# Kernel optimization log

Hardware: AMD Instinct MI355X
Metric: run time of the kernel (lower is better)

The kernel has to match this reference:

```python
import jax, jax.numpy as jnp
import numpy as np

B, T, V = 256, 40, 5000
D, Z, L = 512, 128, 2


def setup_inputs() -> dict:
    key = jax.random.key(0)
    ks = jax.random.split(key, 10)
    s = 0.05  # weight scale to keep gates unsaturated
    return {
        "z": jax.random.normal(ks[0], (B, Z), jnp.float32),
        "x": jax.random.randint(ks[1], (B, T), 0, V),
        "emb": jax.random.normal(ks[2], (V, D), jnp.float32) * s,
        "Wg0": jax.random.normal(ks[3], (4, D, D + Z + D), jnp.float32) * s,
        "bg0": jnp.zeros((4, D), jnp.float32),
        "Wg1": jax.random.normal(ks[4], (4, D, D + D), jnp.float32) * s,
        "bg1": jnp.zeros((4, D), jnp.float32),
        "Wout": jax.random.normal(ks[5], (V, D + Z), jnp.float32) * s,
        "bout": jnp.zeros((V,), jnp.float32),
        "tw1": jax.random.normal(ks[6], (L, 4 * D, Z), jnp.float32) * s,
        "tb1": jnp.zeros((L, 4 * D), jnp.float32),
        "tw2": jax.random.normal(ks[7], (L, 2 * D, 4 * D), jnp.float32) * s,
        "tb2": jnp.zeros((L, 2 * D), jnp.float32),
    }


def reference(z, x, emb, Wg0, bg0, Wg1, bg1, Wout, bout, tw1, tb1, tw2, tb2):
    b, d = z.shape[0], emb.shape[1]
    # transformh0: Linear -> ReLU -> Linear -> Tanh, then split into (h0, c0)
    states = []
    for l in range(L):
        hh = jnp.tanh(jax.nn.relu(z @ tw1[l].T + tb1[l]) @ tw2[l].T + tb2[l])
        hh = hh.reshape(b, 2, d)
        states.append((hh[:, 0], hh[:, 1]))
    states = tuple(states)

    emb_x = emb[x]  # [B, T, D]
    Ws, bs = (Wg0, Wg1), (bg0, bg1)

    def cell(xin, h, c, W, bb):
        hx = jnp.concatenate([h, xin], axis=-1)  # Gate cats [h, input]
        g = jnp.einsum('bf,gdf->bgd', hx, W) + bb  # fused 4 gate GEMMs
        i = jax.nn.sigmoid(g[:, 0])
        f = jax.nn.sigmoid(g[:, 1])
        o = jax.nn.sigmoid(g[:, 2])
        cn = jnp.tanh(g[:, 3])
        c = f * c + i * cn
        return o * jnp.tanh(c), c

    def multi(xin, states):
        H = jnp.zeros((b, d), xin.dtype)
        new, cur = [], xin
        for l in range(L):
            h, c = cell(cur, states[l][0], states[l][1], Ws[l], bs[l])
            H = H + h
            new.append((h, c))
            cur = h
        return H, tuple(new)

    h_t, states = multi(jnp.concatenate([emb_x[:, 0], z], axis=-1), states)

    def step(carry, inp):
        h_t, states = carry
        e_i, x_i = inp
        logits = jnp.concatenate([h_t, z], axis=-1) @ Wout.T + bout
        lp = jax.nn.log_softmax(logits, axis=-1)
        lp_i = jnp.take_along_axis(lp, x_i[:, None], axis=-1)  # [B,1]
        h_t, states = multi(jnp.concatenate([e_i, z], axis=-1), states)
        return (h_t, states), lp_i

    xs = (jnp.swapaxes(emb_x[:, 1:], 0, 1), x[:, 1:].T)
    _, lps = jax.lax.scan(step, (h_t, states), xs)
    # cumsum over time then take last == sum over steps -> [B, 1]
    return jnp.sum(lps, axis=0)
```

## Files before the change

kernel.cpp:

```cpp
#include <hip/hip_runtime.h>


typedef unsigned int uint;
typedef unsigned short ushort;
typedef unsigned long long u64;
typedef __attribute__((ext_vector_type(8))) __bf16 bf16x8;
typedef __attribute__((ext_vector_type(4))) float f32x4;
typedef __attribute__((ext_vector_type(8))) ushort ushort8v;

#define OFF_CNT 0L
#define OFF_W0  4096L
#define OFF_W1  4722688L
#define OFF_WO  8916992L
#define OFF_EFT 15470592L
#define OFF_ZFT 25956352L
#define OFF_TW1 26021888L
#define OFF_TW2 27070464L
#define OFF_GB  35459072L
#define OFF_C0  40701952L
#define OFF_C1  41226240L
#define OFF_MB  41750528L
#define OFF_SB  41914368L
#define OFF_TGT 42078208L
#define OFF_H0S 42205184L
#define OFF_H1S 52690944L
#define OFF_HSS 63176704L

#define HPAR 262144L
#define HMT  131072L
#define SLOT_G 24576
#define SLOT_L 32768


__device__ __forceinline__ uint ald32(const uint* p) {
  return __hip_atomic_load(p, __ATOMIC_RELAXED, __HIP_MEMORY_SCOPE_AGENT);
}
__device__ __forceinline__ void ast32(uint* p, uint v) {
  __hip_atomic_store(p, v, __ATOMIC_RELAXED, __HIP_MEMORY_SCOPE_AGENT);
}
__device__ __forceinline__ float aldf(const float* p) {
  return __hip_atomic_load(p, __ATOMIC_RELAXED, __HIP_MEMORY_SCOPE_AGENT);
}
__device__ __forceinline__ void astf(float* p, float v) {
  __hip_atomic_store(p, v, __ATOMIC_RELAXED, __HIP_MEMORY_SCOPE_AGENT);
}
__device__ __forceinline__ void ast64(u64* p, u64 v) {
  __hip_atomic_store(p, v, __ATOMIC_RELAXED, __HIP_MEMORY_SCOPE_AGENT);
}

__device__ __forceinline__ void postS(uint* s, uint v) {
  __syncthreads();
  if (threadIdx.x == 0) ast32(s, v);
}

__device__ __forceinline__ void gateM(const uint* S, int n, u64 need, uint tgt, uint& vc) {
  if (threadIdx.x < 64) {
    const int li = threadIdx.x;
    uint v = (li < n) ? vc : 0xffffffffu;
    int r = 0;
    for (;;) {
      if ((__ballot((int)(v >= tgt)) & need) == need) break;
      if (li < n && v < tgt) v = ald32(S + li);
      if ((__ballot((int)(v >= tgt)) & need) == need) break;
      if (r < 2) __builtin_amdgcn_s_sleep(1);
      else if (r < 5) __builtin_amdgcn_s_sleep(4);
      else __builtin_amdgcn_s_sleep(8);
      ++r;
    }
    if (li < n) vc = v;
  }
  asm volatile("" ::: "memory");
  __builtin_amdgcn_s_barrier();
  asm volatile("" ::: "memory");
}

__device__ __forceinline__ ushort f2bf(float f) {
  uint u = __float_as_uint(f);
  u = (u + 0x7fffu + ((u >> 16) & 1u)) >> 16;
  return (ushort)u;
}
__device__ __forceinline__ float bf2f(ushort u) { return __uint_as_float(((uint)u) << 16); }
__device__ __forceinline__ float sigm(float v) { return 1.f / (1.f + __expf(-v)); }
__device__ __forceinline__ float tanh_f(float v) {
  float a = fabsf(v);
  float e = __expf(-2.f * a);
  return copysignf((1.f - e) / (1.f + e), v);
}
__device__ __forceinline__ f32x4 mfma16(bf16x8 a, bf16x8 b, f32x4 c) {
  return __builtin_amdgcn_mfma_f32_16x16x32_bf16(a, b, c, 0, 0, 0);
}

__device__ __forceinline__ long fta(int b, int k, int KC) {
  return ((long)(((b >> 7) & 1) * KC + (k >> 5)) << 12) +
         (((((b >> 4) & 7) << 2) + ((k >> 3) & 3)) << 7) + ((b & 15) << 3) + (k & 7);
}

__device__ __forceinline__ void gl_lds16(const char* g, char* l) {
  __builtin_amdgcn_global_load_lds((const __attribute__((address_space(1))) void*)g,
                                   (__attribute__((address_space(3))) void*)l, 16, 0, 0);
}

__device__ __forceinline__ void stageA4(const char* A, char* dst, int o) {
#pragma unroll
  for (int i = 0; i < 4; ++i) gl_lds16(A + i * 4096 + o, dst + i * 4096 + o);
}
__device__ __forceinline__ void stage_gB(int bsec, const char* Bs, char* dst, int o) {
  const char* B = Bs + (long)bsec * 8192;
#pragma unroll
  for (int i = 0; i < 2; ++i) gl_lds16(B + i * 4096 + o, dst + 16384 + i * 4096 + o);
}
__device__ __forceinline__ void stage_lB(int bsec, const char* Blo, const char* Bhi, char* dst,
                                         int o) {
  const char* bl = Blo + (long)bsec * 8192;
  const char* bh = Bhi + (long)bsec * 8192;
#pragma unroll
  for (int i = 0; i < 2; ++i) gl_lds16(bl + i * 4096 + o, dst + 16384 + i * 4096 + o);
#pragma unroll
  for (int i = 0; i < 2; ++i) gl_lds16(bh + i * 4096 + o, dst + 24576 + i * 4096 + o);
}

__device__ __forceinline__ void gw3(int r) {
  if (r <= 0) __builtin_amdgcn_s_waitcnt(0x0F70);
  else if (r == 1) __builtin_amdgcn_s_waitcnt(0x0F76);
  else if (r == 2) __builtin_amdgcn_s_waitcnt(0x0F7C);
  else __builtin_amdgcn_s_waitcnt(0x4F72);
}
__device__ __forceinline__ void lw2(int r) {
  if (r <= 0) __builtin_amdgcn_s_waitcnt(0x0F70);
  else if (r == 1) __builtin_amdgcn_s_waitcnt(0x0F78);
  else __builtin_amdgcn_s_waitcnt(0x4F70);
}
__device__ __forceinline__ void gvw16(int s) {
  if (s == 0) __builtin_amdgcn_s_waitcnt(0x4F78);
  else if (s <= 12) __builtin_amdgcn_s_waitcnt(0x4F72);
  else if (s == 13) __builtin_amdgcn_s_waitcnt(0x0F7C);
  else if (s == 14) __builtin_amdgcn_s_waitcnt(0x0F76);
  else __builtin_amdgcn_s_waitcnt(0x0F70);
}

__device__ __forceinline__ void gemm_chunk_g(const char* sb, int ab, int bb, f32x4 (&acc)[4][2]) {
#pragma unroll
  for (int c = 0; c < 2; ++c) {
    const char* ap = sb + c * 8192 + ab;
    const char* bp = sb + c * 4096 + bb;
    bf16x8 Af0 = *(const bf16x8*)(ap);
    bf16x8 Af1 = *(const bf16x8*)(ap + 1024);
    bf16x8 Af2 = *(const bf16x8*)(ap + 2048);
    bf16x8 Af3 = *(const bf16x8*)(ap + 3072);
    bf16x8 Bf0 = *(const bf16x8*)(bp);
    bf16x8 Bf1 = *(const bf16x8*)(bp + 1024);
    acc[0][0] = mfma16(Af0, Bf0, acc[0][0]);
    acc[0][1] = mfma16(Af0, Bf1, acc[0][1]);
    acc[1][0] = mfma16(Af1, Bf0, acc[1][0]);
    acc[1][1] = mfma16(Af1, Bf1, acc[1][1]);
    acc[2][0] = mfma16(Af2, Bf0, acc[2][0]);
    acc[2][1] = mfma16(Af2, Bf1, acc[2][1]);
    acc[3][0] = mfma16(Af3, Bf0, acc[3][0]);
    acc[3][1] = mfma16(Af3, Bf1, acc[3][1]);
  }
}

__device__ __forceinline__ void gemm_chunk_l(const char* sb, int ab, int bb, f32x4 (&acc)[4][4]) {
#pragma unroll
  for (int c = 0; c < 2; ++c) {
    const char* ap = sb + c * 8192 + ab;
    const char* bp = sb + c * 4096 + bb;
    bf16x8 Af[4], Bf[4];
#pragma unroll
    for (int m = 0; m < 4; ++m) Af[m] = *(const bf16x8*)(ap + m * 1024);
#pragma unroll
    for (int n = 0; n < 4; ++n) Bf[n] = *(const bf16x8*)(bp + n * 1024);
#pragma unroll
    for (int m = 0; m < 4; ++m)
#pragma unroll
      for (int n = 0; n < 4; ++n) acc[m][n] = mfma16(Af[m], Bf[n], acc[m][n]);
  }
}

__device__ __forceinline__ void phaseL8(const char* A0, const char* Blo, const char* Bhi,
                                        char* smem, int o, int ab, int bb, f32x4 (&acc)[4][4]) {
#pragma unroll
  for (int p = 0; p < 4; ++p) {
    char* d = smem + p * SLOT_L;
    stageA4(A0 + (long)p * 16384, d, o);
    stage_lB(p, Blo, Bhi, d, o);
  }
#pragma unroll
  for (int s = 0; s < 8; ++s) {
    if (s == 0) __builtin_amdgcn_s_waitcnt(0x4F78);
    else if (s <= 5) __builtin_amdgcn_s_waitcnt(0x4F70);
    else if (s == 6) __builtin_amdgcn_s_waitcnt(0x0F78);
    else __builtin_amdgcn_s_waitcnt(0x0F70);
    __builtin_amdgcn_s_barrier();
    if (s >= 1 && s <= 4) {
      const int sn = s + 3;
      char* d = smem + (sn % 4) * SLOT_L;
      stageA4(A0 + (long)sn * 16384, d, o);
      stage_lB(sn, Blo, Bhi, d, o);
    }
    gemm_chunk_l(smem + (s % 4) * SLOT_L, ab, bb, acc);
  }
  __builtin_amdgcn_s_barrier();
}

__device__ __forceinline__ void run_gemm_init(const char* A0, const char* Bs, int S, char* smem,
                                              int tid, int wm, int wn, int lane,
                                              f32x4 (&acc)[4][2]) {
  const int o = tid * 16;
  const int D = S < 4 ? S : 4;
  for (int s = 0; s < D; ++s) {
    char* d = smem + s * SLOT_G;
    stageA4(A0 + (long)s * 16384, d, o);
    stage_gB(s, Bs, d, o);
  }
  const int ab = wm * 4096 + lane * 16;
  const int bb = 16384 + wn * 2048 + lane * 16;
  for (int s = 0; s < S; ++s) {
    const int rem = S - 1 - s;
    gw3(rem < 3 ? rem : 3);
    __builtin_amdgcn_s_barrier();
    char* sb = smem + (s % 5) * SLOT_G;
    if (s + 4 < S) {
      char* d = smem + ((s + 4) % 5) * SLOT_G;
      stageA4(A0 + (long)(s + 4) * 16384, d, o);
      stage_gB(s + 4, Bs, d, o);
    }
    gemm_chunk_g(sb, ab, bb, acc);
  }
  __syncthreads();
}

__device__ __forceinline__ void store_lds_tile(float* lds, f32x4 (&acc)[4][2], int wm, int wn,
                                               int lane) {
  const int l15 = lane & 15, lq = lane >> 4;
#pragma unroll
  for (int m = 0; m < 4; ++m)
#pragma unroll
    for (int n = 0; n < 2; ++n)
#pragma unroll
      for (int r = 0; r < 4; ++r)
        lds[(wm * 64 + m * 16 + lq * 4 + r) * 68 + (wn * 32 + n * 16 + l15)] = acc[m][n][r];
}
__device__ __forceinline__ void store_lds_tile128(float* lds, f32x4 (&acc)[4][4], int wm, int wn,
                                                  int lane) {
  const int l15 = lane & 15, lq = lane >> 4;
#pragma unroll
  for (int m = 0; m < 4; ++m)
#pragma unroll
    for (int n = 0; n < 4; ++n)
#pragma unroll
      for (int r = 0; r < 4; ++r)
        lds[(wm * 64 + m * 16 + lq * 4 + r) * 132 + (wn * 64 + n * 16 + l15)] = acc[m][n][r];
}

template <bool WHS>
__device__ __forceinline__ void gates_pw4(const float* tile, int tid, int b0, int d0,
                                          const float* __restrict__ bg, float (&cp)[8],
                                          ushort* __restrict__ hw, const uint (&h0p)[4],
                                          ushort* __restrict__ hs) {
#pragma unroll
  for (int jj = 0; jj < 4; ++jj) {
    const int pi = tid + jj * 256;
    const int bl = pi >> 3, e = pi & 7;
    const f32x4 g0 = ((const f32x4*)tile)[bl * 17 + 2 * e];
    const f32x4 g1 = ((const f32x4*)tile)[bl * 17 + 2 * e + 1];
    const int d = d0 + 2 * e, b = b0 + bl;
    float h2[2];
#pragma unroll
    for (int u = 0; u < 2; ++u) {
      const f32x4 g = u ? g1 : g0;
      const int dd = d + u;
      const float ii = sigm(g[0] + bg[dd]);
      const float ff = sigm(g[1] + bg[512 + dd]);
      const float oo = sigm(g[2] + bg[1024 + dd]);
      const float cn = tanh_f(g[3] + bg[1536 + dd]);
      const float c = ff * cp[jj * 2 + u] + ii * cn;
      cp[jj * 2 + u] = c;
      h2[u] = oo * tanh_f(c);
    }
    const long ft = fta(b, d, 16);
    ast32((uint*)(hw + ft), (uint)f2bf(h2[0]) | ((uint)f2bf(h2[1]) << 16));
    if (WHS) {
      const uint h0v = h0p[jj];
      const float s0 = h2[0] + bf2f((ushort)(h0v & 0xffffu));
      const float s1 = h2[1] + bf2f((ushort)(h0v >> 16));
      ast32((uint*)(hs + ft), (uint)f2bf(s0) | ((uint)f2bf(s1) << 16));
    }
  }
}

__device__ __forceinline__ float combine_row4(const float* __restrict__ MBc,
                                              const float* __restrict__ SBc,
                                              const float* __restrict__ TGTc, int r, int lane) {
  float M = lane < 40 ? aldf(&MBc[r * 40 + lane]) : -3.0e38f;
  float S = lane < 40 ? aldf(&SBc[r * 40 + lane]) : 0.f;
#pragma unroll
  for (int off = 32; off > 0; off >>= 1) {
    const float Mo = __shfl_xor(M, off, 64);
    const float So = __shfl_xor(S, off, 64);
    const float Mn = fmaxf(M, Mo);
    S = S * __expf(M - Mn) + So * __expf(Mo - Mn);
    M = Mn;
  }
  return aldf(&TGTc[r]) - (M + __logf(S));
}

__device__ __forceinline__ void cv8(ushort8v& o, const float* s) {
  const f32x4 a = *(const f32x4*)s, b = *(const f32x4*)(s + 4);
#pragma unroll
  for (int j = 0; j < 4; ++j) o[j] = f2bf(a[j]);
#pragma unroll
  for (int j = 0; j < 4; ++j) o[4 + j] = f2bf(b[j]);
}
__device__ __forceinline__ void bft8(ushort* dst, int col, int kg, int KC, const float* src) {
  ushort8v o;
  cv8(o, src);
  *(ushort8v*)(dst + ((long)((col >> 6) * KC + (kg >> 2)) << 11) +
               (((((col >> 4) & 3) << 2) + (kg & 3)) << 7) + ((col & 15) << 3)) = o;
}
__device__ __forceinline__ void bft8z(ushort* dst, int col, int kg, int KC) {
  ushort8v o = (ushort8v)0;
  *(ushort8v*)(dst + ((long)((col >> 6) * KC + (kg >> 2)) << 11) +
               (((((col >> 4) & 3) << 2) + (kg & 3)) << 7) + ((col & 15) << 3)) = o;
}
__device__ __forceinline__ void aft8(ushort* dst, int b, int kg, int KC, const float* src) {
  ushort8v o;
  cv8(o, src);
  *(ushort8v*)(dst + ((long)(((b >> 7) & 1) * KC + (kg >> 2)) << 12) +
               (((((b >> 4) & 7) << 2) + (kg & 3)) << 7) + ((b & 15) << 3)) = o;
}

__global__ void __launch_bounds__(256) prep_kernel(
    const float* __restrict__ Wg0, const float* __restrict__ Wg1, const float* __restrict__ Wout,
    const float* __restrict__ emb, const float* __restrict__ z, const int* __restrict__ x,
    const float* __restrict__ tw1, const float* __restrict__ tw2, unsigned char* __restrict__ ws) {
  ushort* W0 = (ushort*)(ws + OFF_W0);
  ushort* W1 = (ushort*)(ws + OFF_W1);
  ushort* WO = (ushort*)(ws + OFF_WO);
  ushort* EF = (ushort*)(ws + OFF_EFT);
  ushort* ZF = (ushort*)(ws + OFF_ZFT);
  ushort* T1 = (ushort*)(ws + OFF_TW1);
  ushort* T2 = (ushort*)(ws + OFF_TW2);
  const long N0 = 294912, N1 = 262144, N2 = 409600, N3 = 655360, N4 = 4096, N5 = 65536,
             N6 = 524288;
  const long total = N0 + N1 + N2 + N3 + N4 + N5 + N6;
  for (long idx = (long)blockIdx.x * 256 + threadIdx.x; idx < total;
       idx += (long)gridDim.x * 256) {
    long j = idx;
    if (j < N0) {
      const int col = (int)(j / 144), kg = (int)(j - (long)col * 144);
      bft8(W0, col, kg, 36, Wg0 + (long)((col & 3) * 512 + (col >> 2)) * 1152 + kg * 8);
    } else if ((j -= N0) < N1) {
      const int col = (int)(j >> 7), kg = (int)(j & 127);
      bft8(W1, col, kg, 32, Wg1 + (long)((col & 3) * 512 + (col >> 2)) * 1024 + kg * 8);
    } else if ((j -= N1) < N2) {
      const int col = (int)(j / 80), kg = (int)(j - (long)col * 80);
      if (col < 5000)
        bft8(WO, col, kg, 20, Wout + (long)col * 640 + kg * 8);
      else
        bft8z(WO, col, kg, 20);
    } else if ((j -= N2) < N3) {
      const int t = (int)(j >> 14), r = (int)(j & 16383);
      const int b = r >> 6, kg = r & 63;
      aft8(EF + (long)t * 131072, b, kg, 16, emb + (long)x[b * 40 + t] * 512 + kg * 8);
    } else if ((j -= N3) < N4) {
      const int b = (int)(j >> 4), kg = (int)(j & 15);
      aft8(ZF, b, kg, 4, z + b * 128 + kg * 8);
    } else if ((j -= N4) < N5) {
      const int col = (int)(j >> 4), kg = (int)(j & 15);
      bft8(T1, col, kg, 4, tw1 + (long)(col >> 11) * 262144 + (long)(col & 2047) * 128 + kg * 8);
    } else {
      j -= N5;
      const int col = (int)(j >> 8), kg = (int)(j & 255);
      bft8(T2, col, kg, 64, tw2 + (long)(col >> 10) * 2097152 + (long)(col & 1023) * 2048 + kg * 8);
    }
  }
}

__global__ void __launch_bounds__(256) decoder_main(
    const int* __restrict__ x, const float* __restrict__ bg0, const float* __restrict__ bg1,
    const float* __restrict__ bout, const float* __restrict__ tb1, const float* __restrict__ tb2,
    unsigned char* __restrict__ ws, float* __restrict__ out) {
  __shared__ __align__(16) char smem[157696];

  uint* CNT = (uint*)(ws + OFF_CNT);

  const char* cW0 = (const char*)(ws + OFF_W0);
  const char* cW1 = (const char*)(ws + OFF_W1);
  const char* cWO = (const char*)(ws + OFF_WO);
  const char* cEF = (const char*)(ws + OFF_EFT);
  const char* cZF = (const char*)(ws + OFF_ZFT);
  const char* cT1 = (const char*)(ws + OFF_TW1);
  const char* cT2 = (const char*)(ws + OFF_TW2);
  char* cGB = (char*)(ws + OFF_GB);
  char* cH0S = (char*)(ws + OFF_H0S);
  char* cH1S = (char*)(ws + OFF_H1S);
  char* cHSS = (char*)(ws + OFF_HSS);
  float* C0f = (float*)(ws + OFF_C0);
  float* C1f = (float*)(ws + OFF_C1);
  float* MBf = (float*)(ws + OFF_MB);
  float* SBf = (float*)(ws + OFF_SB);
  float* TGTf = (float*)(ws + OFF_TGT);

  const int bid = blockIdx.x;
  const int tid = threadIdx.x;
  const int lane = tid & 63;
  const int w = tid >> 6;
  const int wm = w & 1, wn = w >> 1;
  const int xcd = bid & 7;
  const int slot = bid >> 3;
  const int o16 = tid * 16;

  int role, mt_r = 0, idx = 0;
  if (xcd < 2) {
    role = 0; mt_r = xcd; idx = slot;
  } else if (xcd < 4) {
    role = 1; mt_r = xcd - 2; idx = slot;
  } else if (xcd < 6) {
    role = 2; mt_r = xcd - 4; idx = slot;
  } else if (slot < 8) {
    role = 2; mt_r = xcd - 6; idx = 32 + slot;
  } else if (slot < 24) {
    role = 3; idx = (xcd - 6) * 16 + (slot - 8); mt_r = idx >> 4;
  } else {
    return;
  }

  const int ab = wm * 4096 + lane * 16;
  const int bbg = 16384 + wn * 2048 + lane * 16;
  const int bbl = 16384 + wn * 8192 + lane * 16;
  float* EPI = (float*)(smem + 122880);

  float cpriv[8];
  float accO0 = 0.f, accO1 = 0.f;

  if (bid < 128) {
    const int i_mt = bid & 1, i_ng = bid >> 1;
    f32x4 acc[4][2];
#pragma unroll
    for (int m = 0; m < 4; ++m)
#pragma unroll
      for (int n = 0; n < 2; ++n) acc[m][n] = (f32x4){0.f, 0.f, 0.f, 0.f};
    run_gemm_init(cZF + (long)i_mt * 32768, cT1 + (long)i_ng * 16384, 2, smem, tid, wm, wn,
                  lane, acc);
    store_lds_tile(EPI, acc, wm, wn, lane);
    __syncthreads();
    const int b0i = i_mt * 128, n0i = i_ng * 64;
    ushort* GBu = (ushort*)cGB;
    for (int i = tid; i < 2048; i += 256) {
      const int bl = i >> 4, q = i & 15;
      const f32x4 v = ((const f32x4*)EPI)[bl * 17 + q];
      const int cb = n0i + q * 4;
      const int l = cb >> 11, rr = cb & 2047;
      u64 pk = 0;
#pragma unroll
      for (int cc = 0; cc < 4; ++cc) pk |= (u64)f2bf(fmaxf(v[cc] + tb1[cb + cc], 0.f)) << (cc * 16);
      ast64((u64*)(GBu + (long)l * 524288 + fta(b0i + bl, rr, 64)), pk);
    }
    postS(CNT + 512 + bid, 1u);
  }

  if (bid < 64) {
    uint ca = 0, cb2 = 0;
    gateM(CNT + 512, 64, ~0ull, 1u, ca);
    gateM(CNT + 576, 64, ~0ull, 1u, cb2);
    const int i_mt = bid & 1, i_ng = bid >> 1;
    const int l = i_ng >> 4;
    f32x4 acc[4][2];
#pragma unroll
    for (int m = 0; m < 4; ++m)
#pragma unroll
      for (int n = 0; n < 2; ++n) acc[m][n] = (f32x4){0.f, 0.f, 0.f, 0.f};
    run_gemm_init(cGB + (long)l * 1048576 + (long)i_mt * 524288, cT2 + (long)i_ng * 262144, 32,
                  smem, tid, wm, wn, lane, acc);
    store_lds_tile(EPI, acc, wm, wn, lane);
    __syncthreads();
    const int b0i = i_mt * 128, n0i = i_ng * 64;
    for (int i = tid; i < 2048; i += 256) {
      const int bl = i >> 4, q = i & 15;
      const f32x4 v = ((const f32x4*)EPI)[bl * 17 + q];
      const int cb = n0i + q * 4;
      const int ll = cb >> 10, rr = cb & 1023;
      const int b = b0i + bl;
      if (rr < 512) {
        u64 pk = 0;
#pragma unroll
        for (int cc = 0; cc < 4; ++cc) pk |= (u64)f2bf(tanh_f(v[cc] + tb2[cb + cc])) << (cc * 16);
        ast64((u64*)((ushort*)(ll ? cH1S : cH0S) + fta(b, rr, 16)), pk);
      } else {
        float* Cf = (ll ? C1f : C0f) + b * 512 + (rr - 512);
#pragma unroll
        for (int cc = 0; cc < 4; ++cc) astf(Cf + cc, tanh_f(v[cc] + tb2[cb + cc]));
      }
    }
    postS(CNT + 640 + bid, 1u);
  }

  if (role == 0) {
    const int mt = mt_r, g = idx;
    uint* SH0m = CNT + mt * 64;
    const char* Az = cZF + (long)mt * 32768;
    const char* Bs = cW0 + (long)g * 147456;
    f32x4 pz0[4][2];
#pragma unroll
    for (int m = 0; m < 4; ++m)
#pragma unroll
      for (int n = 0; n < 2; ++n) pz0[m][n] = (f32x4){0.f, 0.f, 0.f, 0.f};
    run_gemm_init(Az, Bs + 131072, 2, smem, tid, wm, wn, lane, pz0);
    uint cI2 = 0, ch0 = 0;
    gateM(CNT + 640, 64, ~0ull, 1u, cI2);
#pragma unroll
    for (int jj = 0; jj < 4; ++jj) {
      const int pi = tid + jj * 256, bl = pi >> 3, e = pi & 7;
      cpriv[jj * 2 + 0] = aldf(&C0f[(mt * 128 + bl) * 512 + g * 16 + 2 * e]);
      cpriv[jj * 2 + 1] = aldf(&C0f[(mt * 128 + bl) * 512 + g * 16 + 2 * e + 1]);
    }
    uint dum[4] = {0, 0, 0, 0};
    for (int t = 0; t < 39; ++t) {
      const char* Ae = cEF + (long)t * HPAR + (long)mt * HMT;
      const char* Ah = cH0S + (long)t * HPAR + (long)mt * HMT;
      if (t >= 1) gateM(SH0m, 32, 0xFFFFFFFFull, (uint)t, ch0);
      f32x4 acc[4][2];
#pragma unroll
      for (int m = 0; m < 4; ++m)
#pragma unroll
        for (int n = 0; n < 2; ++n) acc[m][n] = pz0[m][n];
#pragma unroll
      for (int p = 0; p < 5; ++p) {
        char* d = smem + p * SLOT_G;
        stageA4(Ae + (long)p * 16384, d, o16);
        stage_gB(8 + p, Bs, d, o16);
      }
      for (int s = 0; s < 16; ++s) {
        gvw16(s);
        __builtin_amdgcn_s_barrier();
        const int sn = s + 4;
        if (s >= 1 && sn < 16) {
          char* d = smem + (sn % 5) * SLOT_G;
          if (sn < 8) {
            stageA4(Ae + (long)sn * 16384, d, o16);
            stage_gB(8 + sn, Bs, d, o16);
          } else {
            stageA4(Ah + (long)(sn - 8) * 16384, d, o16);
            stage_gB(sn - 8, Bs, d, o16);
          }
        }
        gemm_chunk_g(smem + (s % 5) * SLOT_G, ab, bbg, acc);
      }
      store_lds_tile(EPI, acc, wm, wn, lane);
      __syncthreads();
      gates_pw4<false>(EPI, tid, mt * 128, g * 16, bg0, cpriv,
                       (ushort*)(cH0S + (long)(t + 1) * HPAR), dum, nullptr);
      postS(&SH0m[g], (uint)(t + 1));
    }
  } else if (role == 1) {
    const int mt = mt_r, g = idx;
    uint* SH0m = CNT + mt * 64;
    uint* SH1m = CNT + 128 + mt * 64;
    const char* Bs = cW1 + (long)g * 131072;
    uint cI2 = 0, ch1 = 0, ch0 = 0;
    gateM(CNT + 640, 64, ~0ull, 1u, cI2);
#pragma unroll
    for (int jj = 0; jj < 4; ++jj) {
      const int pi = tid + jj * 256, bl = pi >> 3, e = pi & 7;
      cpriv[jj * 2 + 0] = aldf(&C1f[(mt * 128 + bl) * 512 + g * 16 + 2 * e]);
      cpriv[jj * 2 + 1] = aldf(&C1f[(mt * 128 + bl) * 512 + g * 16 + 2 * e + 1]);
    }
    for (int t = 0; t < 39; ++t) {
      const char* Ah1 = cH1S + (long)t * HPAR + (long)mt * HMT;
      const char* Ah0 = cH0S + (long)(t + 1) * HPAR + (long)mt * HMT;
      if (t >= 1) gateM(SH1m, 32, 0xFFFFFFFFull, (uint)t, ch1);
      gateM(SH0m, 32, 0xFFFFFFFFull, (uint)(t + 1), ch0);
      f32x4 acc[4][2];
#pragma unroll
      for (int m = 0; m < 4; ++m)
#pragma unroll
        for (int n = 0; n < 2; ++n) acc[m][n] = (f32x4){0.f, 0.f, 0.f, 0.f};
#pragma unroll
      for (int p = 0; p < 5; ++p) {
        char* d = smem + p * SLOT_G;
        stageA4(Ah1 + (long)p * 16384, d, o16);
        stage_gB(p, Bs, d, o16);
      }
      for (int s = 0; s < 16; ++s) {
        gvw16(s);
        __builtin_amdgcn_s_barrier();
        const int sn = s + 4;
        if (s >= 1 && sn < 16) {
          char* d = smem + (sn % 5) * SLOT_G;
          const char* A = sn < 8 ? Ah1 + (long)sn * 16384 : Ah0 + (long)(sn - 8) * 16384;
          stageA4(A, d, o16);
          stage_gB(sn, Bs, d, o16);
        }
        gemm_chunk_g(smem + (s % 5) * SLOT_G, ab, bbg, acc);
      }
      uint h0p[4];
      {
        const ushort* h0r = (const ushort*)(cH0S + (long)(t + 1) * HPAR);
#pragma unroll
        for (int jj = 0; jj < 4; ++jj) {
          const int pi = tid + jj * 256, bl = pi >> 3, e = pi & 7;
          h0p[jj] = *(const uint*)(h0r + fta(mt * 128 + bl, g * 16 + 2 * e, 16));
        }
      }
      store_lds_tile(EPI, acc, wm, wn, lane);
      __syncthreads();
      gates_pw4<true>(EPI, tid, mt * 128, g * 16, bg1, cpriv,
                      (ushort*)(cH1S + (long)(t + 1) * HPAR), h0p,
                      (ushort*)(cHSS + (long)t * HPAR));
      postS(&SH1m[g], (uint)(t + 1));
    }
  } else if (role == 2) {
    const int lmt = mt_r, lng = idx;
    uint* SH1m = CNT + 128 + lmt * 64;
    uint* SLGm = CNT + 256 + lmt * 64;
    uint* SCBm = CNT + 384 + lmt * 64;
    const char* Blo = cWO + (long)(2 * lng) * 81920;
    const char* Bhi = cWO + (long)(2 * lng + 1) * 81920;
    const char* Az = cZF + (long)lmt * 32768;
    f32x4 pz[4][4];
#pragma unroll
    for (int m = 0; m < 4; ++m)
#pragma unroll
      for (int n = 0; n < 4; ++n) pz[m][n] = (f32x4){0.f, 0.f, 0.f, 0.f};
#pragma unroll
    for (int p = 0; p < 2; ++p) {
      char* d = smem + p * SLOT_L;
      stageA4(Az + (long)p * 16384, d, o16);
      stage_lB(8 + p, Blo, Bhi, d, o16);
    }
    for (int s = 0; s < 2; ++s) {
      lw2(1 - s);
      __builtin_amdgcn_s_barrier();
      gemm_chunk_l(smem + s * SLOT_L, ab, bbl, pz);
    }
    __syncthreads();
    {
      const int l15 = lane & 15;
#pragma unroll
      for (int n = 0; n < 4; ++n) {
        const int col = lng * 128 + wn * 64 + n * 16 + l15;
        const float bb = col < 5000 ? bout[col] : -3.0e38f;
#pragma unroll
        for (int m = 0; m < 4; ++m)
#pragma unroll
          for (int r = 0; r < 4; ++r) pz[m][n][r] += bb;
      }
    }
    uint ch1 = 0, ccb = 0;
    for (int t = 0; t < 39; ++t) {
      const char* Ahs = cHSS + (long)t * HPAR + (long)lmt * HMT;
      if (t >= 4) gateM(SCBm, 16, 0xFFFFull, (uint)(t - 3), ccb);
      gateM(SH1m, 32, 0xFFFFFFFFull, (uint)(t + 1), ch1);
      f32x4 acc[4][4];
#pragma unroll
      for (int m = 0; m < 4; ++m)
#pragma unroll
        for (int n = 0; n < 4; ++n) acc[m][n] = pz[m][n];
      phaseL8(Ahs, Blo, Bhi, smem, o16, ab, bbl, acc);
      __syncthreads();
      store_lds_tile128((float*)smem, acc, wm, wn, lane);
      __syncthreads();
      const int row = tid >> 1, half = tid & 1, b = lmt * 128 + row;
      const int n0 = lng * 128 + half * 64;
      const int xt = x[b * 40 + t + 1];
      const float* rowp = (const float*)smem + row * 132 + half * 64;
      float mx = -3.0e38f, tv = 0.f;
      for (int j = 0; j < 64; j += 4) {
        const f32x4 v = *(const f32x4*)(rowp + j);
#pragma unroll
        for (int cc = 0; cc < 4; ++cc) {
          mx = fmaxf(mx, v[cc]);
          if (n0 + j + cc == xt) tv = v[cc];
        }
      }
      float sa = 0.f;
      for (int j = 0; j < 64; j += 4) {
        const f32x4 v = *(const f32x4*)(rowp + j);
#pragma unroll
        for (int cc = 0; cc < 4; ++cc) sa += __expf(v[cc] - mx);
      }
      const float mo = __shfl_xor(mx, 1, 64), so = __shfl_xor(sa, 1, 64),
                  to = __shfl_xor(tv, 1, 64);
      const float Mn = fmaxf(mx, mo);
      const float Sm = sa * __expf(mx - Mn) + so * __expf(mo - Mn);
      const int sl = t & 3;
      if (half == 0) {
        astf(&MBf[sl * 10240 + b * 40 + lng], Mn);
        astf(&SBf[sl * 10240 + b * 40 + lng], Sm);
        if (xt >= lng * 128 && xt < lng * 128 + 128) astf(&TGTf[sl * 256 + b], tv + to);
      }
      postS(&SLGm[lng], (uint)(t + 1));
    }
  } else {
    const int cb = idx;
    const int cmt = mt_r;
    uint* SLGm = CNT + 256 + cmt * 64;
    uint* SCBm = CNT + 384 + cmt * 64;
    const int r0 = cb * 8 + w * 2;
    uint clg = 0;
    for (int t = 0; t < 39; ++t) {
      gateM(SLGm, 40, (1ull << 40) - 1, (uint)(t + 1), clg);
      const int sl = t & 3;
      accO0 += combine_row4(MBf + sl * 10240, SBf + sl * 10240, TGTf + sl * 256, r0, lane);
      accO1 += combine_row4(MBf + sl * 10240, SBf + sl * 10240, TGTf + sl * 256, r0 + 1, lane);
      postS(&SCBm[cb & 15], (uint)(t + 1));
    }
    if (lane == 0) {
      out[r0] = accO0;
      out[r0 + 1] = accO1;
    }
  }
}

extern "C" void kernel_launch(void* const* d_in, const int* in_sizes, int n_in, void* d_out,
                              int out_size, void* d_ws, size_t ws_size, hipStream_t stream) {
  const float* z = (const float*)d_in[0];
  const int* x = (const int*)d_in[1];
  const float* emb = (const float*)d_in[2];
  const float* Wg0 = (const float*)d_in[3];
  const float* bg0 = (const float*)d_in[4];
  const float* Wg1 = (const float*)d_in[5];
  const float* bg1 = (const float*)d_in[6];
  const float* Wout = (const float*)d_in[7];
  const float* bout = (const float*)d_in[8];
  const float* tw1 = (const float*)d_in[9];
  const float* tb1 = (const float*)d_in[10];
  const float* tw2 = (const float*)d_in[11];
  const float* tb2 = (const float*)d_in[12];
  unsigned char* ws = (unsigned char*)d_ws;
  float* out = (float*)d_out;

  hipMemsetAsync(ws, 0, 4096, stream);
  prep_kernel<<<2048, 256, 0, stream>>>(Wg0, Wg1, Wout, emb, z, x, tw1, tw2, ws);
  decoder_main<<<256, 256, 0, stream>>>(x, bg0, bg1, bout, tb1, tb2, ws, out);
}
```

Baseline: 580.6 us.

## Prefetch next timestep's leading GEMM chunks before the epilogue in all roles

Each persistent role (layer-0 cell, layer-1 cell, logits) now issues the first pipeline stages of the next timestep's GEMM (embedding, h0, or hidden-state operands plus weights) right after the current step's accumulators are stored, so those loads overlap the gate or softmax epilogue. Layer 1 reorders its K loop to consume h0 (already ready) before its own recurrent h1, and waits on the h0 flag for the next step early. The logits role inlines its pipelined loop and waits for the next h1 before prefetching. In exchange, the epilogue has to share memory bandwidth with the prefetch, and the early waits on cross-block flags could stall producers or expose hazards if a slot is reused while still being read.

```diff
diff --git a/kernel.cpp b/kernel.cpp
--- a/kernel.cpp
+++ b/kernel.cpp
@@ -137,6 +137,12 @@
   else if (s == 14) __builtin_amdgcn_s_waitcnt(0x0F76);
   else __builtin_amdgcn_s_waitcnt(0x0F70);
 }
+__device__ __forceinline__ void lvw8(int s) {
+  if (s == 0) __builtin_amdgcn_s_waitcnt(0x4F78);
+  else if (s <= 5) __builtin_amdgcn_s_waitcnt(0x4F70);
+  else if (s == 6) __builtin_amdgcn_s_waitcnt(0x0F78);
+  else __builtin_amdgcn_s_waitcnt(0x0F70);
+}
 
 __device__ __forceinline__ void gemm_chunk_g(const char* sb, int ab, int bb, f32x4 (&acc)[4][2]) {
 #pragma unroll
@@ -175,32 +181,6 @@
 #pragma unroll
       for (int n = 0; n < 4; ++n) acc[m][n] = mfma16(Af[m], Bf[n], acc[m][n]);
   }
-}
-
-__device__ __forceinline__ void phaseL8(const char* A0, const char* Blo, const char* Bhi,
-                                        char* smem, int o, int ab, int bb, f32x4 (&acc)[4][4]) {
-#pragma unroll
-  for (int p = 0; p < 4; ++p) {
-    char* d = smem + p * SLOT_L;
-    stageA4(A0 + (long)p * 16384, d, o);
-    stage_lB(p, Blo, Bhi, d, o);
-  }
-#pragma unroll
-  for (int s = 0; s < 8; ++s) {
-    if (s == 0) __builtin_amdgcn_s_waitcnt(0x4F78);
-    else if (s <= 5) __builtin_amdgcn_s_waitcnt(0x4F70);
-    else if (s == 6) __builtin_amdgcn_s_waitcnt(0x0F78);
-    else __builtin_amdgcn_s_waitcnt(0x0F70);
-    __builtin_amdgcn_s_barrier();
-    if (s >= 1 && s <= 4) {
-      const int sn = s + 3;
-      char* d = smem + (sn % 4) * SLOT_L;
-      stageA4(A0 + (long)sn * 16384, d, o);
-      stage_lB(sn, Blo, Bhi, d, o);
-    }
-    gemm_chunk_l(smem + (s % 4) * SLOT_L, ab, bb, acc);
-  }
-  __builtin_amdgcn_s_barrier();
 }
 
 __device__ __forceinline__ void run_gemm_init(const char* A0, const char* Bs, int S, char* smem,
@@ -516,6 +496,15 @@
       cpriv[jj * 2 + 1] = aldf(&C0f[(mt * 128 + bl) * 512 + g * 16 + 2 * e + 1]);
     }
     uint dum[4] = {0, 0, 0, 0};
+    {
+      const char* Ae0 = cEF + (long)mt * HMT;
+#pragma unroll
+      for (int p = 0; p < 5; ++p) {
+        char* d = smem + p * SLOT_G;
+        stageA4(Ae0 + (long)p * 16384, d, o16);
+        stage_gB(8 + p, Bs, d, o16);
+      }
+    }
     for (int t = 0; t < 39; ++t) {
       const char* Ae = cEF + (long)t * HPAR + (long)mt * HMT;
       const char* Ah = cH0S + (long)t * HPAR + (long)mt * HMT;
@@ -525,12 +514,6 @@
       for (int m = 0; m < 4; ++m)
 #pragma unroll
         for (int n = 0; n < 2; ++n) acc[m][n] = pz0[m][n];
-#pragma unroll
-      for (int p = 0; p < 5; ++p) {
-        char* d = smem + p * SLOT_G;
-        stageA4(Ae + (long)p * 16384, d, o16);
-        stage_gB(8 + p, Bs, d, o16);
-      }
       for (int s = 0; s < 16; ++s) {
         gvw16(s);
         __builtin_amdgcn_s_barrier();
@@ -549,6 +532,15 @@
       }
       store_lds_tile(EPI, acc, wm, wn, lane);
       __syncthreads();
+      if (t + 1 < 39) {
+        const char* Aen = cEF + (long)(t + 1) * HPAR + (long)mt * HMT;
+#pragma unroll
+        for (int p = 0; p < 5; ++p) {
+          char* d = smem + p * SLOT_G;
+          stageA4(Aen + (long)p * 16384, d, o16);
+          stage_gB(8 + p, Bs, d, o16);
+        }
+      }
       gates_pw4<false>(EPI, tid, mt * 128, g * 16, bg0, cpriv,
                        (ushort*)(cH0S + (long)(t + 1) * HPAR), dum, nullptr);
       postS(&SH0m[g], (uint)(t + 1));
@@ -566,45 +558,62 @@
       cpriv[jj * 2 + 0] = aldf(&C1f[(mt * 128 + bl) * 512 + g * 16 + 2 * e]);
       cpriv[jj * 2 + 1] = aldf(&C1f[(mt * 128 + bl) * 512 + g * 16 + 2 * e + 1]);
     }
-    for (int t = 0; t < 39; ++t) {
-      const char* Ah1 = cH1S + (long)t * HPAR + (long)mt * HMT;
-      const char* Ah0 = cH0S + (long)(t + 1) * HPAR + (long)mt * HMT;
-      if (t >= 1) gateM(SH1m, 32, 0xFFFFFFFFull, (uint)t, ch1);
-      gateM(SH0m, 32, 0xFFFFFFFFull, (uint)(t + 1), ch0);
-      f32x4 acc[4][2];
-#pragma unroll
-      for (int m = 0; m < 4; ++m)
-#pragma unroll
-        for (int n = 0; n < 2; ++n) acc[m][n] = (f32x4){0.f, 0.f, 0.f, 0.f};
+    gateM(SH0m, 32, 0xFFFFFFFFull, 1u, ch0);
+    {
+      const char* Ah0i = cH0S + 1L * HPAR + (long)mt * HMT;
 #pragma unroll
       for (int p = 0; p < 5; ++p) {
         char* d = smem + p * SLOT_G;
-        stageA4(Ah1 + (long)p * 16384, d, o16);
-        stage_gB(p, Bs, d, o16);
-      }
+        stageA4(Ah0i + (long)p * 16384, d, o16);
+        stage_gB(8 + p, Bs, d, o16);
+      }
+    }
+    for (int t = 0; t < 39; ++t) {
+      const char* Ah0 = cH0S + (long)(t + 1) * HPAR + (long)mt * HMT;
+      const char* Ah1 = cH1S + (long)t * HPAR + (long)mt * HMT;
+      if (t >= 1) gateM(SH1m, 32, 0xFFFFFFFFull, (uint)t, ch1);
+      uint h0p[4];
+      {
+        const ushort* h0r = (const ushort*)(cH0S + (long)(t + 1) * HPAR);
+#pragma unroll
+        for (int jj = 0; jj < 4; ++jj) {
+          const int pi = tid + jj * 256, bl = pi >> 3, e = pi & 7;
+          h0p[jj] = *(const uint*)(h0r + fta(mt * 128 + bl, g * 16 + 2 * e, 16));
+        }
+      }
+      f32x4 acc[4][2];
+#pragma unroll
+      for (int m = 0; m < 4; ++m)
+#pragma unroll
+        for (int n = 0; n < 2; ++n) acc[m][n] = (f32x4){0.f, 0.f, 0.f, 0.f};
       for (int s = 0; s < 16; ++s) {
         gvw16(s);
         __builtin_amdgcn_s_barrier();
         const int sn = s + 4;
         if (s >= 1 && sn < 16) {
           char* d = smem + (sn % 5) * SLOT_G;
-          const char* A = sn < 8 ? Ah1 + (long)sn * 16384 : Ah0 + (long)(sn - 8) * 16384;
-          stageA4(A, d, o16);
-          stage_gB(sn, Bs, d, o16);
+          if (sn < 8) {
+            stageA4(Ah0 + (long)sn * 16384, d, o16);
+            stage_gB(8 + sn, Bs, d, o16);
+          } else {
+            stageA4(Ah1 + (long)(sn - 8) * 16384, d, o16);
+            stage_gB(sn - 8, Bs, d, o16);
+          }
         }
         gemm_chunk_g(smem + (s % 5) * SLOT_G, ab, bbg, acc);
       }
-      uint h0p[4];
-      {
-        const ushort* h0r = (const ushort*)(cH0S + (long)(t + 1) * HPAR);
-#pragma unroll
-        for (int jj = 0; jj < 4; ++jj) {
-          const int pi = tid + jj * 256, bl = pi >> 3, e = pi & 7;
-          h0p[jj] = *(const uint*)(h0r + fta(mt * 128 + bl, g * 16 + 2 * e, 16));
-        }
-      }
       store_lds_tile(EPI, acc, wm, wn, lane);
       __syncthreads();
+      if (t + 1 < 39) {
+        gateM(SH0m, 32, 0xFFFFFFFFull, (uint)(t + 2), ch0);
+        const char* Ah0n = cH0S + (long)(t + 2) * HPAR + (long)mt * HMT;
+#pragma unroll
+        for (int p = 0; p < 5; ++p) {
+          char* d = smem + p * SLOT_G;
+          stageA4(Ah0n + (long)p * 16384, d, o16);
+          stage_gB(8 + p, Bs, d, o16);
+        }
+      }
       gates_pw4<true>(EPI, tid, mt * 128, g * 16, bg1, cpriv,
                       (ushort*)(cH1S + (long)(t + 1) * HPAR), h0p,
                       (ushort*)(cHSS + (long)t * HPAR));
@@ -648,6 +657,16 @@
       }
     }
     uint ch1 = 0, ccb = 0;
+    gateM(SH1m, 32, 0xFFFFFFFFull, 1u, ch1);
+    {
+      const char* Ahs0 = cHSS + (long)lmt * HMT;
+#pragma unroll
+      for (int p = 0; p < 4; ++p) {
+        char* d = smem + p * SLOT_L;
+        stageA4(Ahs0 + (long)p * 16384, d, o16);
+        stage_lB(p, Blo, Bhi, d, o16);
+      }
+    }
     for (int t = 0; t < 39; ++t) {
       const char* Ahs = cHSS + (long)t * HPAR + (long)lmt * HMT;
       if (t >= 4) gateM(SCBm, 16, 0xFFFFull, (uint)(t - 3), ccb);
@@ -657,8 +676,18 @@
       for (int m = 0; m < 4; ++m)
 #pragma unroll
         for (int n = 0; n < 4; ++n) acc[m][n] = pz[m][n];
-      phaseL8(Ahs, Blo, Bhi, smem, o16, ab, bbl, acc);
-      __syncthreads();
+      for (int s = 0; s < 8; ++s) {
+        lvw8(s);
+        __builtin_amdgcn_s_barrier();
+        const int sn = s + 3;
+        if (s >= 1 && sn < 8) {
+          char* d = smem + (sn & 3) * SLOT_L;
+          stageA4(Ahs + (long)sn * 16384, d, o16);
+          stage_lB(sn, Blo, Bhi, d, o16);
+        }
+        gemm_chunk_l(smem + (s & 3) * SLOT_L, ab, bbl, acc);
+      }
+      __builtin_amdgcn_s_barrier();
       store_lds_tile128((float*)smem, acc, wm, wn, lane);
       __syncthreads();
       const int row = tid >> 1, half = tid & 1, b = lmt * 128 + row;
@@ -689,6 +718,17 @@
         astf(&MBf[sl * 10240 + b * 40 + lng], Mn);
         astf(&SBf[sl * 10240 + b * 40 + lng], Sm);
         if (xt >= lng * 128 && xt < lng * 128 + 128) astf(&TGTf[sl * 256 + b], tv + to);
+      }
+      __syncthreads();
+      if (t + 1 < 39) {
+        gateM(SH1m, 32, 0xFFFFFFFFull, (uint)(t + 2), ch1);
+        const char* Ahsn = cHSS + (long)(t + 1) * HPAR + (long)lmt * HMT;
+#pragma unroll
+        for (int p = 0; p < 4; ++p) {
+          char* d = smem + p * SLOT_L;
+          stageA4(Ahsn + (long)p * 16384, d, o16);
+          stage_lB(p, Blo, Bhi, d, o16);
+        }
       }
       postS(&SLGm[lng], (uint)(t + 1));
     }
```

Result: slower. 617.0 us (+6.3%).
